# Performance work log

Hardware: AMD Instinct MI355X
Metric: run time of the kernel (lower is better)

## Reference

```python
import jax, jax.numpy as jnp
import numpy as np
import math

B, T, F, H = 8, 1024, 512, 8
DK = F // H

def setup_inputs() -> dict:
    key = jax.random.key(0)
    ks = jax.random.split(key, 14)
    s = 0.02
    return {
        "query": jax.random.normal(ks[0], (B, T, F), jnp.float32),
        "key_in": jax.random.normal(ks[1], (B, T, F), jnp.float32),
        "value": jax.random.normal(ks[2], (B, T, F), jnp.float32),
        "pos_emb": jax.random.normal(ks[3], (1, 2 * T - 1, F), jnp.float32),
        "mask": jnp.ones((B, 1, T), jnp.int32),
        "Wq": jax.random.normal(ks[4], (F, F), jnp.float32) * s,
        "bq": jnp.zeros((F,), jnp.float32),
        "Wk": jax.random.normal(ks[5], (F, F), jnp.float32) * s,
        "bk": jnp.zeros((F,), jnp.float32),
        "Wv": jax.random.normal(ks[6], (F, F), jnp.float32) * s,
        "bv": jnp.zeros((F,), jnp.float32),
        "Wo": jax.random.normal(ks[7], (F, F), jnp.float32) * s,
        "bo": jnp.zeros((F,), jnp.float32),
        "Wp": jax.random.normal(ks[8], (F, F), jnp.float32) * s,
        "pos_bias_u": jax.random.normal(ks[9], (H, DK), jnp.float32) * s,
        "pos_bias_v": jax.random.normal(ks[10], (H, DK), jnp.float32) * s,
    }

def _rel_shift(x):
    # x: [B,H,T1, 2*T1-1] -> Transformer-XL pad/reshape trick -> [B,H,T1,T1]
    b, h, t1, n = x.shape
    zero_pad = jnp.zeros((b, h, t1, 1), x.dtype)
    x_padded = jnp.concatenate([zero_pad, x], axis=-1)  # [B,H,T1,n+1]
    x_padded = x_padded.reshape(b, h, n + 1, t1)
    x = x_padded[:, :, 1:].reshape(b, h, t1, n)
    return x[..., : n // 2 + 1]

def reference(query, key_in, value, pos_emb, mask,
              Wq, bq, Wk, bk, Wv, bv, Wo, bo, Wp, pos_bias_u, pos_bias_v):
    b, t1, f = query.shape
    # qkv projections -> [B,T,H,DK]
    q = (query @ Wq.T + bq).reshape(b, t1, H, DK)
    k = (key_in @ Wk.T + bk).reshape(b, -1, H, DK)
    v = (value @ Wv.T + bv).reshape(b, -1, H, DK)
    # positional projection (batch 1) -> [P,H,DK]
    p = (pos_emb @ Wp.T).reshape(pos_emb.shape[1], H, DK)
    q_u = q + pos_bias_u  # broadcast [H,DK]
    q_v = q + pos_bias_v
    matrix_ac = jnp.einsum("bthd,bshd->bhts", q_u, k)
    matrix_bd = jnp.einsum("bthd,phd->bhtp", q_v, p)
    matrix_bd = _rel_shift(matrix_bd)
    scores = (matrix_ac + matrix_bd) / math.sqrt(DK)  # [B,H,T,T]
    neg = jnp.finfo(scores.dtype).min
    m = (mask[:, None, :, :] == 0)  # [B,1,1,T] or [B,1,T,T]
    scores = jnp.where(m, neg, scores)
    attn = jax.nn.softmax(scores, axis=-1)
    attn = jnp.where(m, 0.0, attn)
    x = jnp.einsum("bhts,bshd->bthd", attn, v).reshape(b, t1, H * DK)
    return x @ Wo.T + bo
```

## Files before the change

### kernel.cpp

```cpp
#include <hip/hip_runtime.h>
#include <math.h>

#define T_SEQ 1024
#define FEAT  512
#define NH    8
#define DKH   64

typedef __attribute__((ext_vector_type(8))) short          bf16x8;
typedef _Float16 f16;
typedef __attribute__((ext_vector_type(8))) _Float16       f16x8;
typedef __attribute__((ext_vector_type(4))) float          f32x4;
typedef __attribute__((ext_vector_type(8))) unsigned short u16x8;
typedef __attribute__((ext_vector_type(4))) unsigned short u16x4;

__device__ __forceinline__ float bf2f(unsigned short u) {
    union { unsigned int i; float f; } x; x.i = ((unsigned int)u) << 16; return x.f;
}
__device__ __forceinline__ unsigned short f2bf(float f) {
    union { float f; unsigned int i; } x; x.f = f;
    unsigned int r = x.i + 0x7FFFu + ((x.i >> 16) & 1u);
    return (unsigned short)(r >> 16);
}
__device__ __forceinline__ unsigned short f2h_bits(float f) {
    const f16 h = (f16)f;
    union { f16 h; unsigned short u; } x; x.h = h; return x.u;
}

struct WSplit {
    const float*    src[5];
    unsigned short* hi[5];
    unsigned short* lo[5];
};

__global__ __launch_bounds__(256)
void split_weights(WSplit pk) {
    const int ten = blockIdx.y;
    const float4* s = (const float4*)pk.src[ten];
    u16x4* dh = (u16x4*)pk.hi[ten];
    u16x4* dl = (u16x4*)pk.lo[ten];
    const int n4 = FEAT * FEAT / 4;
    for (int i = blockIdx.x * blockDim.x + threadIdx.x; i < n4;
         i += gridDim.x * blockDim.x) {
        const float4 v = s[i];
        float a[4] = {v.x, v.y, v.z, v.w};
        u16x4 h, l;
#pragma unroll
        for (int j = 0; j < 4; ++j) {
            h[j] = f2bf(a[j]);
            l[j] = f2bf(a[j] - bf2f(h[j]));
        }
        dh[i] = h; dl[i] = l;
    }
}

template<int OUTMODE>
__global__ __launch_bounds__(256)
void gemm_split(const float* __restrict__ A,
                const unsigned short* __restrict__ Wh,
                const unsigned short* __restrict__ Wl,
                const float* __restrict__ bias,
                void* __restrict__ Cout, int M, int N, int K)
{
    __shared__ unsigned short Ah[64][40];
    __shared__ unsigned short Al[64][40];
    __shared__ unsigned short Bh[64][40];
    __shared__ unsigned short Bl[64][40];

    const int tid  = threadIdx.x;
    const int w    = tid >> 6, lane = tid & 63, g = lane >> 4, c = lane & 15;
    const int m0   = blockIdx.x * 64, n0 = blockIdx.y * 64;
    const int wr   = (w >> 1) * 32, wc = (w & 1) * 32;
    const int r0   = tid >> 2, ch = tid & 3;

    f32x4 acc[2][2];
#pragma unroll
    for (int m = 0; m < 2; ++m)
#pragma unroll
        for (int n = 0; n < 2; ++n)
#pragma unroll
            for (int r = 0; r < 4; ++r) acc[m][n][r] = 0.f;

    float4 ar[2];
    u16x8  brh, brl;
    auto ldA = [&](int kc) {
        const int gr = m0 + r0;
        if (gr < M) {
            const size_t base = (size_t)gr * K + kc * 32 + ch * 8;
            ar[0] = *(const float4*)&A[base];
            ar[1] = *(const float4*)&A[base + 4];
        } else {
            ar[0] = make_float4(0.f, 0.f, 0.f, 0.f);
            ar[1] = make_float4(0.f, 0.f, 0.f, 0.f);
        }
    };
    auto ldB = [&](int kc) {
        const size_t base = (size_t)(n0 + r0) * K + kc * 32 + ch * 8;
        brh = *(const u16x8*)&Wh[base];
        brl = *(const u16x8*)&Wl[base];
    };

    ldA(0); ldB(0);

    const int nk = K / 32;
    for (int kc = 0; kc < nk; ++kc) {
        __syncthreads();
        {
            float v[8] = {ar[0].x, ar[0].y, ar[0].z, ar[0].w,
                          ar[1].x, ar[1].y, ar[1].z, ar[1].w};
            u16x8 h, l;
#pragma unroll
            for (int j = 0; j < 8; ++j) {
                h[j] = f2bf(v[j]);
                l[j] = f2bf(v[j] - bf2f(h[j]));
            }
            *(u16x8*)&Ah[r0][ch * 8] = h;
            *(u16x8*)&Al[r0][ch * 8] = l;
            *(u16x8*)&Bh[r0][ch * 8] = brh;
            *(u16x8*)&Bl[r0][ch * 8] = brl;
        }
        __syncthreads();
        if (kc + 1 < nk) { ldA(kc + 1); ldB(kc + 1); }

        bf16x8 ah[2], al[2], bh[2], bl[2];
#pragma unroll
        for (int m = 0; m < 2; ++m) {
            ah[m] = *(const bf16x8*)&Ah[wr + 16 * m + c][8 * g];
            al[m] = *(const bf16x8*)&Al[wr + 16 * m + c][8 * g];
        }
#pragma unroll
        for (int n = 0; n < 2; ++n) {
            bh[n] = *(const bf16x8*)&Bh[wc + 16 * n + c][8 * g];
            bl[n] = *(const bf16x8*)&Bl[wc + 16 * n + c][8 * g];
        }
#pragma unroll
        for (int m = 0; m < 2; ++m)
#pragma unroll
            for (int n = 0; n < 2; ++n) {
                acc[m][n] = __builtin_amdgcn_mfma_f32_16x16x32_bf16(ah[m], bh[n], acc[m][n], 0, 0, 0);
                acc[m][n] = __builtin_amdgcn_mfma_f32_16x16x32_bf16(ah[m], bl[n], acc[m][n], 0, 0, 0);
                acc[m][n] = __builtin_amdgcn_mfma_f32_16x16x32_bf16(al[m], bh[n], acc[m][n], 0, 0, 0);
            }
    }

#pragma unroll
    for (int n = 0; n < 2; ++n) {
        const int gcol = n0 + wc + 16 * n + c;
        const float bb = bias ? bias[gcol] : 0.f;
#pragma unroll
        for (int m = 0; m < 2; ++m) {
            if (OUTMODE == 2) {
                const int grb = m0 + wr + 16 * m + 4 * g;
                const int bidx = grb >> 10, t = grb & 1023;
                u16x4 pk4;
#pragma unroll
                for (int r = 0; r < 4; ++r) pk4[r] = f2h_bits(acc[m][n][r] + bb);
                *(u16x4*)&((unsigned short*)Cout)[((size_t)(bidx * FEAT + gcol)) * T_SEQ + t] = pk4;
            } else {
#pragma unroll
                for (int r = 0; r < 4; ++r) {
                    const int gr = m0 + wr + 16 * m + 4 * g + r;
                    if (gr < M) {
                        const float v = acc[m][n][r] + bb;
                        if (OUTMODE == 0) ((float*)Cout)[(size_t)gr * N + gcol] = v;
                        else ((unsigned short*)Cout)[(size_t)gr * N + gcol] = f2h_bits(v);
                    }
                }
            }
        }
    }
}

#define AST  72
#define BDST 132

__global__ __launch_bounds__(256)
void attn_f16(const unsigned short* __restrict__ qb,
              const unsigned short* __restrict__ kb,
              const unsigned short* __restrict__ vtg,
              const unsigned short* __restrict__ pb,
              const int* __restrict__ mask,
              const float* __restrict__ pbu, const float* __restrict__ pbv,
              float* __restrict__ xout)
{
    extern __shared__ unsigned short sm[];
    unsigned short* kt  = sm;
    unsigned short* vtT = kt  + 64 * AST;
    unsigned short* pt  = vtT + 64 * AST;
    unsigned short* ps  = pt  + 128 * AST;
    unsigned short* bdb = ps  + 64 * AST;
    f16* bdf = (f16*)bdb;
    f16* psf = (f16*)ps;

    const int tid = threadIdx.x;
    const int w = tid >> 6, lane = tid & 63, g = lane >> 4, c = lane & 15;
    const int t0 = blockIdx.x * 64;
    const int b  = blockIdx.y >> 3, h = blockIdx.y & 7;

    const unsigned short* ksrc = kb + ((size_t)b * T_SEQ) * FEAT + h * DKH;
    const unsigned short* vsrc = vtg + ((size_t)(b * FEAT + h * DKH)) * T_SEQ;
    const unsigned short* psrc = pb + h * DKH;

    f16x8 aq0, aq1, av0, av1;
    {
        const unsigned short* qp =
            qb + ((size_t)(b * T_SEQ + t0 + 16 * w + c)) * FEAT + h * DKH + 8 * g;
        const f16x8 q0 = *(const f16x8*)qp;
        const f16x8 q1 = *(const f16x8*)(qp + 32);
        const float* pu = pbu + h * DKH + 8 * g;
        const float* pv = pbv + h * DKH + 8 * g;
#pragma unroll
        for (int j = 0; j < 8; ++j) {
            const float f0 = (float)q0[j], f1 = (float)q1[j];
            aq0[j] = (f16)(f0 + pu[j]);       av0[j] = (f16)(f0 + pv[j]);
            aq1[j] = (f16)(f1 + pu[j + 32]);  av1[j] = (f16)(f1 + pv[j + 32]);
        }
    }

    f32x4 accO[4];
    float m_r[4], l_r[4];
#pragma unroll
    for (int n = 0; n < 4; ++n)
#pragma unroll
        for (int r = 0; r < 4; ++r) accO[n][r] = 0.f;
#pragma unroll
    for (int r = 0; r < 4; ++r) { m_r[r] = -3.0e38f; l_r[r] = 0.f; }

    for (int st = 0; st < 16; ++st) {
        const int s0 = st * 64;
        const int pbase = (T_SEQ - DKH) - t0 + s0;
        __syncthreads();
#pragma unroll
        for (int q2 = 0; q2 < 2; ++q2) {
            const int id = tid + 256 * q2, row = id >> 3, chq = id & 7;
            *(u16x8*)&kt[row * AST + chq * 8] =
                *(const u16x8*)&ksrc[(size_t)(s0 + row) * FEAT + chq * 8];
            *(u16x8*)&vtT[row * AST + chq * 8] =
                *(const u16x8*)&vsrc[(size_t)row * T_SEQ + s0 + chq * 8];
        }
#pragma unroll
        for (int q2 = 0; q2 < 4; ++q2) {
            const int id = tid + 256 * q2, prow = id >> 3, chq = id & 7;
            u16x8 p8;
            if (prow < 127)
                p8 = *(const u16x8*)&psrc[(size_t)(pbase + prow) * FEAT + chq * 8];
            else {
#pragma unroll
                for (int j = 0; j < 8; ++j) p8[j] = 0;
            }
            *(u16x8*)&pt[prow * AST + chq * 8] = p8;
        }
        __syncthreads();

        f32x4 acS[4];
#pragma unroll
        for (int j = 0; j < 4; ++j)
#pragma unroll
            for (int r = 0; r < 4; ++r) acS[j][r] = 0.f;
#pragma unroll
        for (int j = 0; j < 4; ++j) {
            const f16x8 b0 = *(const f16x8*)&kt[(16 * j + c) * AST + 8 * g];
            const f16x8 b1 = *(const f16x8*)&kt[(16 * j + c) * AST + 32 + 8 * g];
            acS[j] = __builtin_amdgcn_mfma_f32_16x16x32_f16(aq0, b0, acS[j], 0, 0, 0);
            acS[j] = __builtin_amdgcn_mfma_f32_16x16x32_f16(aq1, b1, acS[j], 0, 0, 0);
        }

#pragma unroll
        for (int jj = 0; jj < 8; ++jj) {
            f32x4 bda;
#pragma unroll
            for (int r = 0; r < 4; ++r) bda[r] = 0.f;
            const f16x8 b0 = *(const f16x8*)&pt[(16 * jj + c) * AST + 8 * g];
            const f16x8 b1 = *(const f16x8*)&pt[(16 * jj + c) * AST + 32 + 8 * g];
            bda = __builtin_amdgcn_mfma_f32_16x16x32_f16(av0, b0, bda, 0, 0, 0);
            bda = __builtin_amdgcn_mfma_f32_16x16x32_f16(av1, b1, bda, 0, 0, 0);
#pragma unroll
            for (int r = 0; r < 4; ++r)
                bdf[(16 * w + 4 * g + r) * BDST + 16 * jj + c] = (f16)bda[r];
        }
        __syncthreads();

        int mk[4];
#pragma unroll
        for (int j = 0; j < 4; ++j) mk[j] = mask[b * T_SEQ + s0 + 16 * j + c];
#pragma unroll
        for (int r = 0; r < 4; ++r) {
            const int ti = 16 * w + 4 * g + r;
            float sv[4];
#pragma unroll
            for (int j = 0; j < 4; ++j) {
                const float bdv = (float)bdf[ti * BDST + (63 - ti + 16 * j + c)];
                sv[j] = (mk[j] == 0) ? -1.0e30f : (acS[j][r] + bdv) * 0.125f;
            }
            float mx = fmaxf(fmaxf(sv[0], sv[1]), fmaxf(sv[2], sv[3]));
            mx = fmaxf(mx, __shfl_xor(mx, 1)); mx = fmaxf(mx, __shfl_xor(mx, 2));
            mx = fmaxf(mx, __shfl_xor(mx, 4)); mx = fmaxf(mx, __shfl_xor(mx, 8));
            const float mnew = fmaxf(m_r[r], mx);
            const float corr = __expf(m_r[r] - mnew);
            m_r[r] = mnew;
            float rs = 0.f;
#pragma unroll
            for (int j = 0; j < 4; ++j) {
                const float e = (mk[j] == 0) ? 0.f : __expf(sv[j] - mnew);
                rs += e;
                psf[ti * AST + 16 * j + c] = (f16)e;
            }
            rs += __shfl_xor(rs, 1); rs += __shfl_xor(rs, 2);
            rs += __shfl_xor(rs, 4); rs += __shfl_xor(rs, 8);
            l_r[r] = l_r[r] * corr + rs;
#pragma unroll
            for (int n = 0; n < 4; ++n) accO[n][r] *= corr;
        }
        __syncthreads();

        const f16x8 pa0 = *(const f16x8*)&ps[(16 * w + c) * AST + 8 * g];
        const f16x8 pa1 = *(const f16x8*)&ps[(16 * w + c) * AST + 32 + 8 * g];
#pragma unroll
        for (int n = 0; n < 4; ++n) {
            const f16x8 b0 = *(const f16x8*)&vtT[(16 * n + c) * AST + 8 * g];
            const f16x8 b1 = *(const f16x8*)&vtT[(16 * n + c) * AST + 32 + 8 * g];
            accO[n] = __builtin_amdgcn_mfma_f32_16x16x32_f16(pa0, b0, accO[n], 0, 0, 0);
            accO[n] = __builtin_amdgcn_mfma_f32_16x16x32_f16(pa1, b1, accO[n], 0, 0, 0);
        }
    }

#pragma unroll
    for (int r = 0; r < 4; ++r) {
        const float inv = (l_r[r] > 0.f) ? 1.0f / l_r[r] : 0.f;
        const int t = t0 + 16 * w + 4 * g + r;
#pragma unroll
        for (int n = 0; n < 4; ++n)
            xout[((size_t)(b * T_SEQ + t)) * FEAT + h * DKH + 16 * n + c] = accO[n][r] * inv;
    }
}

extern "C" void kernel_launch(void* const* d_in, const int* in_sizes, int n_in,
                              void* d_out, int out_size, void* d_ws, size_t ws_size,
                              hipStream_t stream)
{
    (void)in_sizes; (void)n_in; (void)out_size; (void)ws_size;
    const float* query   = (const float*)d_in[0];
    const float* key_in  = (const float*)d_in[1];
    const float* value   = (const float*)d_in[2];
    const float* pos_emb = (const float*)d_in[3];
    const int*   mask    = (const int*)  d_in[4];
    const float* Wq = (const float*)d_in[5];
    const float* bq = (const float*)d_in[6];
    const float* Wk = (const float*)d_in[7];
    const float* bk = (const float*)d_in[8];
    const float* Wv = (const float*)d_in[9];
    const float* bv = (const float*)d_in[10];
    const float* Wo = (const float*)d_in[11];
    const float* bo = (const float*)d_in[12];
    const float* Wp = (const float*)d_in[13];
    const float* pbu = (const float*)d_in[14];
    const float* pbv = (const float*)d_in[15];
    float* out = (float*)d_out;

    const size_t NTOK = (size_t)8 * T_SEQ;
    char* wsp = (char*)d_ws;
    size_t off = 0;
    auto alloc = [&](size_t bytes) { char* p = wsp + off; off += (bytes + 255) & ~255ull; return p; };

    unsigned short* qbf = (unsigned short*)alloc(NTOK * FEAT * 2);
    unsigned short* kbf = (unsigned short*)alloc(NTOK * FEAT * 2);
    unsigned short* vTb = (unsigned short*)alloc(NTOK * FEAT * 2);
    unsigned short* pbf = (unsigned short*)alloc((size_t)2047 * FEAT * 2);
    float*          xbf = (float*)alloc(NTOK * FEAT * 4);
    unsigned short* wh[5]; unsigned short* wl[5];
    for (int i = 0; i < 5; ++i) {
        wh[i] = (unsigned short*)alloc((size_t)FEAT * FEAT * 2);
        wl[i] = (unsigned short*)alloc((size_t)FEAT * FEAT * 2);
    }

    WSplit sp;
    const float* wsrc[5] = {Wq, Wk, Wv, Wp, Wo};
    for (int i = 0; i < 5; ++i) { sp.src[i] = wsrc[i]; sp.hi[i] = wh[i]; sp.lo[i] = wl[i]; }
    split_weights<<<dim3(64, 5), 256, 0, stream>>>(sp);

    gemm_split<1><<<dim3(128, 8), 256, 0, stream>>>(query,  wh[0], wl[0], bq, qbf, 8192, FEAT, FEAT);
    gemm_split<1><<<dim3(128, 8), 256, 0, stream>>>(key_in, wh[1], wl[1], bk, kbf, 8192, FEAT, FEAT);
    gemm_split<2><<<dim3(128, 8), 256, 0, stream>>>(value,  wh[2], wl[2], bv, vTb, 8192, FEAT, FEAT);
    gemm_split<1><<<dim3(32, 8),  256, 0, stream>>>(pos_emb, wh[3], wl[3], nullptr, pbf, 2047, FEAT, FEAT);

    const int lds_bytes = (64 * AST * 3 + 128 * AST + 64 * BDST) * 2;
    hipFuncSetAttribute((const void*)attn_f16,
                        hipFuncAttributeMaxDynamicSharedMemorySize, lds_bytes);
    attn_f16<<<dim3(16, 64), 256, lds_bytes, stream>>>(qbf, kbf, vTb, pbf,
                                                       mask, pbu, pbv, xbf);

    gemm_split<0><<<dim3(128, 8), 256, 0, stream>>>(xbf, wh[4], wl[4], bo, out, 8192, FEAT, FEAT);
}
```

Measured before the change: 386.9 us.

## Pre-split activations to bf16 hi/lo and stage GEMM tiles via global_load_lds double buffering

```diff
diff --git a/kernel.cpp b/kernel.cpp
--- a/kernel.cpp
+++ b/kernel.cpp
@@ -26,19 +26,26 @@
     union { f16 h; unsigned short u; } x; x.h = h; return x.u;
 }
 
-struct WSplit {
-    const float*    src[5];
-    unsigned short* hi[5];
-    unsigned short* lo[5];
+typedef const __attribute__((address_space(1))) unsigned int* gas_ptr;
+typedef __attribute__((address_space(3))) unsigned int*       las_ptr;
+__device__ __forceinline__ void glds16(const unsigned short* g, unsigned short* l) {
+    __builtin_amdgcn_global_load_lds((gas_ptr)(const void*)g, (las_ptr)(void*)l, 16, 0, 0);
+}
+
+struct SplitPack {
+    const float*    src[9];
+    unsigned short* hi[9];
+    unsigned short* lo[9];
+    int             n4[9];
 };
 
 __global__ __launch_bounds__(256)
-void split_weights(WSplit pk) {
+void split_f32(SplitPack pk) {
     const int ten = blockIdx.y;
+    const int n4  = pk.n4[ten];
     const float4* s = (const float4*)pk.src[ten];
     u16x4* dh = (u16x4*)pk.hi[ten];
     u16x4* dl = (u16x4*)pk.lo[ten];
-    const int n4 = FEAT * FEAT / 4;
     for (int i = blockIdx.x * blockDim.x + threadIdx.x; i < n4;
          i += gridDim.x * blockDim.x) {
         const float4 v = s[i];
@@ -53,93 +60,86 @@
     }
 }
 
+#define GBUF 12288
+
 template<int OUTMODE>
 __global__ __launch_bounds__(256)
-void gemm_split(const float* __restrict__ A,
-                const unsigned short* __restrict__ Wh,
-                const unsigned short* __restrict__ Wl,
-                const float* __restrict__ bias,
-                void* __restrict__ Cout, int M, int N, int K)
+void gemm_ps(const unsigned short* __restrict__ Agh,
+             const unsigned short* __restrict__ Agl,
+             const unsigned short* __restrict__ Wh,
+             const unsigned short* __restrict__ Wl,
+             const float* __restrict__ bias,
+             void* __restrict__ Cout, int M, int N, int K)
 {
-    __shared__ unsigned short Ah[64][40];
-    __shared__ unsigned short Al[64][40];
-    __shared__ unsigned short Bh[64][40];
-    __shared__ unsigned short Bl[64][40];
+    __shared__ unsigned short lds[2 * GBUF];
 
     const int tid  = threadIdx.x;
     const int w    = tid >> 6, lane = tid & 63, g = lane >> 4, c = lane & 15;
-    const int m0   = blockIdx.x * 64, n0 = blockIdx.y * 64;
-    const int wr   = (w >> 1) * 32, wc = (w & 1) * 32;
-    const int r0   = tid >> 2, ch = tid & 3;
-
-    f32x4 acc[2][2];
-#pragma unroll
-    for (int m = 0; m < 2; ++m)
+    const int m0   = blockIdx.x * 128, n0 = blockIdx.y * 64;
+    const int wr   = (w >> 1) * 64, wc = (w & 1) * 32;
+
+    f32x4 acc[4][2];
+#pragma unroll
+    for (int m = 0; m < 4; ++m)
 #pragma unroll
         for (int n = 0; n < 2; ++n)
 #pragma unroll
             for (int r = 0; r < 4; ++r) acc[m][n][r] = 0.f;
 
-    float4 ar[2];
-    u16x8  brh, brl;
-    auto ldA = [&](int kc) {
-        const int gr = m0 + r0;
-        if (gr < M) {
-            const size_t base = (size_t)gr * K + kc * 32 + ch * 8;
-            ar[0] = *(const float4*)&A[base];
-            ar[1] = *(const float4*)&A[base + 4];
-        } else {
-            ar[0] = make_float4(0.f, 0.f, 0.f, 0.f);
-            ar[1] = make_float4(0.f, 0.f, 0.f, 0.f);
+    auto STAGE = [&](unsigned short* base, int kc) {
+        const int k0 = kc * 32;
+#pragma unroll
+        for (int q = 0; q < 2; ++q) {
+            const int chunk = q * 256 + w * 64 + lane;
+            const int row = chunk >> 2, p = chunk & 3;
+            const int gra = m0 + row;
+            const int gr  = (gra < M) ? gra : (M - 1);
+            const size_t go = (size_t)gr * K + k0 + p * 8;
+            glds16(Agh + go, base + chunk * 8);
+            glds16(Agl + go, base + 4096 + chunk * 8);
+        }
+        {
+            const int chunk = w * 64 + lane;
+            const int row = chunk >> 2, p = chunk & 3;
+            const size_t go = (size_t)(n0 + row) * K + k0 + p * 8;
+            glds16(Wh + go, base + 8192 + chunk * 8);
+            glds16(Wl + go, base + 10240 + chunk * 8);
         }
     };
-    auto ldB = [&](int kc) {
-        const size_t base = (size_t)(n0 + r0) * K + kc * 32 + ch * 8;
-        brh = *(const u16x8*)&Wh[base];
-        brl = *(const u16x8*)&Wl[base];
-    };
-
-    ldA(0); ldB(0);
+
+    STAGE(lds, 0);
+    __syncthreads();
 
     const int nk = K / 32;
+    int cur = 0;
     for (int kc = 0; kc < nk; ++kc) {
-        __syncthreads();
-        {
-            float v[8] = {ar[0].x, ar[0].y, ar[0].z, ar[0].w,
-                          ar[1].x, ar[1].y, ar[1].z, ar[1].w};
-            u16x8 h, l;
-#pragma unroll
-            for (int j = 0; j < 8; ++j) {
-                h[j] = f2bf(v[j]);
-                l[j] = f2bf(v[j] - bf2f(h[j]));
-            }
-            *(u16x8*)&Ah[r0][ch * 8] = h;
-            *(u16x8*)&Al[r0][ch * 8] = l;
-            *(u16x8*)&Bh[r0][ch * 8] = brh;
-            *(u16x8*)&Bl[r0][ch * 8] = brl;
-        }
-        __syncthreads();
-        if (kc + 1 < nk) { ldA(kc + 1); ldB(kc + 1); }
-
-        bf16x8 ah[2], al[2], bh[2], bl[2];
-#pragma unroll
-        for (int m = 0; m < 2; ++m) {
-            ah[m] = *(const bf16x8*)&Ah[wr + 16 * m + c][8 * g];
-            al[m] = *(const bf16x8*)&Al[wr + 16 * m + c][8 * g];
+        if (kc + 1 < nk) STAGE(lds + (cur ^ 1) * GBUF, kc + 1);
+
+        const unsigned short* Bs = lds + cur * GBUF;
+        bf16x8 ah[4], al[4], bh[2], bl[2];
+#pragma unroll
+        for (int m = 0; m < 4; ++m) {
+            const int ro = (wr + 16 * m + c) * 32 + g * 8;
+            ah[m] = *(const bf16x8*)&Bs[ro];
+            al[m] = *(const bf16x8*)&Bs[4096 + ro];
         }
 #pragma unroll
         for (int n = 0; n < 2; ++n) {
-            bh[n] = *(const bf16x8*)&Bh[wc + 16 * n + c][8 * g];
-            bl[n] = *(const bf16x8*)&Bl[wc + 16 * n + c][8 * g];
-        }
-#pragma unroll
-        for (int m = 0; m < 2; ++m)
+            const int ro = (wc + 16 * n + c) * 32 + g * 8;
+            bh[n] = *(const bf16x8*)&Bs[8192 + ro];
+            bl[n] = *(const bf16x8*)&Bs[10240 + ro];
+        }
+#pragma unroll
+        for (int m = 0; m < 4; ++m)
 #pragma unroll
             for (int n = 0; n < 2; ++n) {
                 acc[m][n] = __builtin_amdgcn_mfma_f32_16x16x32_bf16(ah[m], bh[n], acc[m][n], 0, 0, 0);
                 acc[m][n] = __builtin_amdgcn_mfma_f32_16x16x32_bf16(ah[m], bl[n], acc[m][n], 0, 0, 0);
                 acc[m][n] = __builtin_amdgcn_mfma_f32_16x16x32_bf16(al[m], bh[n], acc[m][n], 0, 0, 0);
             }
+
+        __syncthreads();
+        cur ^= 1;
     }
 
 #pragma unroll
@@ -147,7 +147,7 @@
         const int gcol = n0 + wc + 16 * n + c;
         const float bb = bias ? bias[gcol] : 0.f;
 #pragma unroll
-        for (int m = 0; m < 2; ++m) {
+        for (int m = 0; m < 4; ++m) {
             if (OUTMODE == 2) {
                 const int grb = m0 + wr + 16 * m + 4 * g;
                 const int bidx = grb >> 10, t = grb & 1023;
@@ -180,7 +180,7 @@
               const unsigned short* __restrict__ pb,
               const int* __restrict__ mask,
               const float* __restrict__ pbu, const float* __restrict__ pbv,
-              float* __restrict__ xout)
+              unsigned short* __restrict__ xh, unsigned short* __restrict__ xl)
 {
     extern __shared__ unsigned short sm[];
     unsigned short* kt  = sm;
@@ -328,8 +328,13 @@
         const float inv = (l_r[r] > 0.f) ? 1.0f / l_r[r] : 0.f;
         const int t = t0 + 16 * w + 4 * g + r;
 #pragma unroll
-        for (int n = 0; n < 4; ++n)
-            xout[((size_t)(b * T_SEQ + t)) * FEAT + h * DKH + 16 * n + c] = accO[n][r] * inv;
+        for (int n = 0; n < 4; ++n) {
+            const float xv = accO[n][r] * inv;
+            const size_t idx = ((size_t)(b * T_SEQ + t)) * FEAT + h * DKH + 16 * n + c;
+            const unsigned short hp = f2bf(xv);
+            xh[idx] = hp;
+            xl[idx] = f2bf(xv - bf2f(hp));
+        }
     }
 }
 
@@ -365,28 +370,43 @@
     unsigned short* kbf = (unsigned short*)alloc(NTOK * FEAT * 2);
     unsigned short* vTb = (unsigned short*)alloc(NTOK * FEAT * 2);
     unsigned short* pbf = (unsigned short*)alloc((size_t)2047 * FEAT * 2);
-    float*          xbf = (float*)alloc(NTOK * FEAT * 4);
     unsigned short* wh[5]; unsigned short* wl[5];
     for (int i = 0; i < 5; ++i) {
         wh[i] = (unsigned short*)alloc((size_t)FEAT * FEAT * 2);
         wl[i] = (unsigned short*)alloc((size_t)FEAT * FEAT * 2);
     }
-
-    WSplit sp;
-    const float* wsrc[5] = {Wq, Wk, Wv, Wp, Wo};
-    for (int i = 0; i < 5; ++i) { sp.src[i] = wsrc[i]; sp.hi[i] = wh[i]; sp.lo[i] = wl[i]; }
-    split_weights<<<dim3(64, 5), 256, 0, stream>>>(sp);
-
-    gemm_split<1><<<dim3(128, 8), 256, 0, stream>>>(query,  wh[0], wl[0], bq, qbf, 8192, FEAT, FEAT);
-    gemm_split<1><<<dim3(128, 8), 256, 0, stream>>>(key_in, wh[1], wl[1], bk, kbf, 8192, FEAT, FEAT);
-    gemm_split<2><<<dim3(128, 8), 256, 0, stream>>>(value,  wh[2], wl[2], bv, vTb, 8192, FEAT, FEAT);
-    gemm_split<1><<<dim3(32, 8),  256, 0, stream>>>(pos_emb, wh[3], wl[3], nullptr, pbf, 2047, FEAT, FEAT);
+    unsigned short* iqh = (unsigned short*)alloc(NTOK * FEAT * 2);
+    unsigned short* iql = (unsigned short*)alloc(NTOK * FEAT * 2);
+    unsigned short* ikh = (unsigned short*)alloc(NTOK * FEAT * 2);
+    unsigned short* ikl = (unsigned short*)alloc(NTOK * FEAT * 2);
+    unsigned short* ivh = (unsigned short*)alloc(NTOK * FEAT * 2);
+    unsigned short* ivl = (unsigned short*)alloc(NTOK * FEAT * 2);
+    unsigned short* iph = (unsigned short*)alloc((size_t)2047 * FEAT * 2);
+    unsigned short* ipl = (unsigned short*)alloc((size_t)2047 * FEAT * 2);
+    unsigned short* xh = iqh;
+    unsigned short* xl = iql;
+
+    SplitPack sp;
+    const float* wsrc[9] = {Wq, Wk, Wv, Wp, Wo, query, key_in, value, pos_emb};
+    unsigned short* hdst[9] = {wh[0], wh[1], wh[2], wh[3], wh[4], iqh, ikh, ivh, iph};
+    unsigned short* ldst[9] = {wl[0], wl[1], wl[2], wl[3], wl[4], iql, ikl, ivl, ipl};
+    for (int i = 0; i < 9; ++i) {
+        sp.src[i] = wsrc[i]; sp.hi[i] = hdst[i]; sp.lo[i] = ldst[i];
+        sp.n4[i] = (i < 5) ? (FEAT * FEAT / 4)
+                           : ((i < 8) ? (int)(NTOK * FEAT / 4) : (2047 * FEAT / 4));
+    }
+    split_f32<<<dim3(256, 9), 256, 0, stream>>>(sp);
+
+    gemm_ps<1><<<dim3(64, 8), 256, 0, stream>>>(iqh, iql, wh[0], wl[0], bq, qbf, 8192, FEAT, FEAT);
+    gemm_ps<1><<<dim3(64, 8), 256, 0, stream>>>(ikh, ikl, wh[1], wl[1], bk, kbf, 8192, FEAT, FEAT);
+    gemm_ps<2><<<dim3(64, 8), 256, 0, stream>>>(ivh, ivl, wh[2], wl[2], bv, vTb, 8192, FEAT, FEAT);
+    gemm_ps<1><<<dim3(16, 8), 256, 0, stream>>>(iph, ipl, wh[3], wl[3], nullptr, pbf, 2047, FEAT, FEAT);
 
     const int lds_bytes = (64 * AST * 3 + 128 * AST + 64 * BDST) * 2;
     hipFuncSetAttribute((const void*)attn_f16,
                         hipFuncAttributeMaxDynamicSharedMemorySize, lds_bytes);
     attn_f16<<<dim3(16, 64), 256, lds_bytes, stream>>>(qbf, kbf, vTb, pbf,
-                                                       mask, pbu, pbv, xbf);
-
-    gemm_split<0><<<dim3(128, 8), 256, 0, stream>>>(xbf, wh[4], wl[4], bo, out, 8192, FEAT, FEAT);
-}
+                                                       mask, pbu, pbv, xh, xl);
+
+    gemm_ps<0><<<dim3(64, 8), 256, 0, stream>>>(xh, xl, wh[4], wl[4], bo, out, 8192, FEAT, FEAT);
+}
```

Measured after the change: 394.4 us. No clear change (+1.9%).
